# Optimization experiments

Hardware: AMD Instinct MI355X
Metric: run time of the kernel (lower is better)

## Reference

```python
import jax, jax.numpy as jnp
import numpy as np

K = 8            # tree arity
DEPTH = 7        # number of levels (0 = root)
N = (K**DEPTH - 1) // (K - 1)   # 299593 nodes, complete K-ary tree
D_EMB = 128
D_ENC = 128
D_DEC = 256


def _build_tree():
    idx = np.arange(N)
    offsets = (K**np.arange(DEPTH + 1) - 1) // (K - 1)  # level start offsets
    levels = np.searchsorted(offsets, idx, side='right') - 1
    parent = np.where(idx > 0, (idx - 1) // K, 0)       # heap layout
    return parent.astype(np.int64), levels.astype(np.int64)


def setup_inputs() -> dict:
    key = jax.random.key(0)
    ks = jax.random.split(key, 8)
    parent, levels = _build_tree()
    s = 0.05
    return {
        'x': jax.random.normal(ks[0], (N, D_EMB), jnp.float32),
        'parent': jnp.asarray(parent),
        'levels': jnp.asarray(levels),
        'num_levels': DEPTH,
        'W_iou': jax.random.normal(ks[1], (D_EMB, 3 * D_ENC), jnp.float32) * s,
        'b_iou': jnp.zeros((3 * D_ENC,), jnp.float32),
        'U_iou': jax.random.normal(ks[2], (D_ENC, 3 * D_ENC), jnp.float32) * s,
        'W_f': jax.random.normal(ks[3], (D_EMB, D_ENC), jnp.float32) * s,
        'b_f': jnp.zeros((D_ENC,), jnp.float32),
        'U_f': jax.random.normal(ks[4], (D_ENC, D_ENC), jnp.float32) * s,
        'W_out': jax.random.normal(ks[5], (D_ENC, D_DEC), jnp.float32) * s,
        'b_out': jnp.zeros((D_DEC,), jnp.float32),
        'ln_gamma': jnp.ones((D_DEC,), jnp.float32),
        'ln_beta': jnp.zeros((D_DEC,), jnp.float32),
    }


def _layer_norm(y, g, b, eps=1e-5):
    mu = jnp.mean(y, axis=-1, keepdims=True)
    var = jnp.var(y, axis=-1, keepdims=True)
    return (y - mu) * jax.lax.rsqrt(var + eps) * g + b


def reference(x, parent, levels, num_levels, W_iou, b_iou, U_iou, W_f, b_f, U_f, W_out, b_out, ln_gamma, ln_beta):
    n = x.shape[0]
    H = U_f.shape[0]
    # precomputed per-node input projections (dropout p=0 -> identity)
    x_iou = x @ W_iou + b_iou       # [N, 3H]
    x_f = x @ W_f + b_f             # [N, H]
    h = jnp.zeros((n, H), x.dtype)
    c = jnp.zeros((n, H), x.dtype)
    Uh_sum = jnp.zeros((n, 3 * H), x.dtype)
    fc_sum = jnp.zeros((n, H), x.dtype)
    # level-synchronous topological propagation: deepest level first
    for l in range(num_levels - 1, -1, -1):
        m = (levels == l)[:, None]
        # apply_node_func for nodes at level l
        iou = x_iou + Uh_sum
        i, o, u = jnp.split(iou, 3, axis=1)
        c_new = jax.nn.sigmoid(i) * jnp.tanh(u) + fc_sum
        h_new = jax.nn.sigmoid(o) * jnp.tanh(c_new)
        c = jnp.where(m, c_new, c)
        h = jnp.where(m, h_new, h)
        if l > 0:
            # message_func + reduce_func: gated child-state sums into parents
            mf = m.astype(x.dtype)
            f = jax.nn.sigmoid(x_f[parent] + h @ U_f)   # f uses dst x_f, src h
            Uh_sum = Uh_sum.at[parent].add((h @ U_iou) * mf)
            fc_sum = fc_sum.at[parent].add((c * f) * mf)
    return jnp.tanh(_layer_norm(h @ W_out + b_out, ln_gamma, ln_beta))
```

## Files before the change

kernel.cpp:

```cpp
#include <hip/hip_runtime.h>
#include <math.h>

#define DEV __device__ __forceinline__

#define NNODES 299593
#define NINTERNAL 37449

typedef __attribute__((ext_vector_type(8))) short short8;
typedef __attribute__((ext_vector_type(4))) float f32x4;

DEV float fsig(float x) { return 1.f / (1.f + __expf(-x)); }
DEV float ftanh(float x) { return 1.f - 2.f / (__expf(2.f * x) + 1.f); }

DEV unsigned short f2bf(float x) {
    unsigned int u = __float_as_uint(x);
    return (unsigned short)((u + 0x7fffu + ((u >> 16) & 1u)) >> 16);
}
DEV float bf2f(unsigned short h) { return __uint_as_float(((unsigned int)h) << 16); }

DEV f32x4 MF(short8 a, short8 b, f32x4 c) {
    return __builtin_amdgcn_mfma_f32_16x16x32_bf16(a, b, c, 0, 0, 0);
}

DEV short8 fragA(const short (*buf)[136], int r, int ks, int g) {
    return *reinterpret_cast<const short8*>(&buf[r][ks * 32 + g * 8]);
}

DEV void load8(float* v, const float* base, long row, int sc, int M) {
    if (row < M) {
        const float4* p4 = reinterpret_cast<const float4*>(base + row * 128 + sc);
        float4 a = p4[0], b = p4[1];
        v[0] = a.x; v[1] = a.y; v[2] = a.z; v[3] = a.w;
        v[4] = b.x; v[5] = b.y; v[6] = b.z; v[7] = b.w;
    } else {
#pragma unroll
        for (int e = 0; e < 8; ++e) v[e] = 0.f;
    }
}

DEV void stageHL(short (*H)[136], short (*L)[136], const float* v, int sr, int sc) {
    short8 vh, vl;
#pragma unroll
    for (int e = 0; e < 8; ++e) {
        unsigned short hb = f2bf(v[e]);
        vh[e] = (short)hb;
        vl[e] = (short)f2bf(v[e] - bf2f(hb));
    }
    *reinterpret_cast<short8*>(&H[sr][sc]) = vh;
    *reinterpret_cast<short8*>(&L[sr][sc]) = vl;
}

struct LvlP {
    const float* x;
    const float* hsum_in;
    const float* fc_in;
    const float* xf_par;
    unsigned short* h_out;
    float* hsum_out;
    float* fc_out;
    const float* Wiou;
    const float* biou;
    const float* Uiou;
    const float* Uf;
    long ntiles;
    int M;
};

template <bool UIOU, bool PAR>
__global__ __launch_bounds__(512) void lvl_kernel(LvlP p) {
    __shared__ __align__(16) short Ah[32][136];
    __shared__ __align__(16) short Al[32][136];
    __shared__ __align__(16) short Sh[UIOU ? 32 : 1][136];
    __shared__ __align__(16) short Sl[UIOU ? 32 : 1][136];
    __shared__ __align__(16) short Hs[32][136];

    const int tid = threadIdx.x;
    const int lane = tid & 63;
    const int w = tid >> 6;
    const int cl = lane & 15;
    const int g = lane >> 4;
    const int sr = tid >> 4;
    const int sc = (tid & 15) * 8;

    short8 Wh[4][3], Wl[4][3], Uh_[4][3], Ufh[4], Ufl[4];
    {
        const int colb = w * 16 + cl;
#pragma unroll
        for (int ks = 0; ks < 4; ++ks) {
#pragma unroll
            for (int f = 0; f < 3; ++f) {
#pragma unroll
                for (int e = 0; e < 8; ++e) {
                    float v = p.Wiou[(ks * 32 + g * 8 + e) * 384 + f * 128 + colb];
                    unsigned short hb = f2bf(v);
                    Wh[ks][f][e] = (short)hb;
                    Wl[ks][f][e] = (short)f2bf(v - bf2f(hb));
                }
                if constexpr (UIOU) {
#pragma unroll
                    for (int e = 0; e < 8; ++e)
                        Uh_[ks][f][e] = (short)f2bf(p.Uiou[(ks * 32 + g * 8 + e) * 384 + f * 128 + colb]);
                }
            }
            if constexpr (PAR) {
#pragma unroll
                for (int e = 0; e < 8; ++e) {
                    float v = p.Uf[(ks * 32 + g * 8 + e) * 128 + colb];
                    unsigned short hb = f2bf(v);
                    Ufh[ks][e] = (short)hb;
                    Ufl[ks][e] = (short)f2bf(v - bf2f(hb));
                }
            }
        }
    }

    long t = blockIdx.x;
    float va[8], sa[8];
    if (t < p.ntiles) {
        load8(va, p.x, t * 32 + sr, sc, p.M);
        if constexpr (UIOU) load8(sa, p.hsum_in, t * 32 + sr, sc, p.M);
    }

    for (; t < p.ntiles; t += gridDim.x) {
        const long row0 = t * 32;

        stageHL(Ah, Al, va, sr, sc);
        if constexpr (UIOU) stageHL(Sh, Sl, sa, sr, sc);
        __syncthreads();

        {
            long tn = t + gridDim.x;
            if (tn < p.ntiles) {
                load8(va, p.x, tn * 32 + sr, sc, p.M);
                if constexpr (UIOU) load8(sa, p.hsum_in, tn * 32 + sr, sc, p.M);
            }
        }

        f32x4 acc[2][3];
#pragma unroll
        for (int rf = 0; rf < 2; ++rf)
#pragma unroll
            for (int f = 0; f < 3; ++f) acc[rf][f] = (f32x4){0.f, 0.f, 0.f, 0.f};

#pragma unroll
        for (int ks = 0; ks < 4; ++ks)
#pragma unroll
            for (int rf = 0; rf < 2; ++rf) {
                short8 ah = fragA(Ah, rf * 16 + cl, ks, g);
                short8 al = fragA(Al, rf * 16 + cl, ks, g);
#pragma unroll
                for (int f = 0; f < 3; ++f) {
                    acc[rf][f] = MF(ah, Wh[ks][f], acc[rf][f]);
                    acc[rf][f] = MF(al, Wh[ks][f], acc[rf][f]);
                    acc[rf][f] = MF(ah, Wl[ks][f], acc[rf][f]);
                }
                if constexpr (UIOU) {
                    short8 sh = fragA(Sh, rf * 16 + cl, ks, g);
                    short8 sl = fragA(Sl, rf * 16 + cl, ks, g);
#pragma unroll
                    for (int f = 0; f < 3; ++f) {
                        acc[rf][f] = MF(sh, Uh_[ks][f], acc[rf][f]);
                        acc[rf][f] = MF(sl, Uh_[ks][f], acc[rf][f]);
                    }
                }
            }

        const int col = w * 16 + cl;
        float hreg[2][4], creg[2][4];
#pragma unroll
        for (int rf = 0; rf < 2; ++rf)
#pragma unroll
            for (int reg = 0; reg < 4; ++reg) {
                const long row = row0 + rf * 16 + g * 4 + reg;
                float hv = 0.f, cv = 0.f;
                if (row < p.M) {
                    float iv = acc[rf][0][reg] + p.biou[col];
                    float ov = acc[rf][1][reg] + p.biou[128 + col];
                    float uv = acc[rf][2][reg] + p.biou[256 + col];
                    float fcv = 0.f;
                    if constexpr (UIOU) fcv = p.fc_in[row * 128 + col];
                    cv = fsig(iv) * ftanh(uv) + fcv;
                    hv = bf2f(f2bf(fsig(ov) * ftanh(cv)));
                }
                hreg[rf][reg] = hv;
                creg[rf][reg] = cv;
                Hs[rf * 16 + g * 4 + reg][col] = (short)f2bf(hv);
            }
        __syncthreads();

        {
            const long row = row0 + sr;
            if (row < p.M)
                *reinterpret_cast<short8*>(p.h_out + row * 128 + sc) =
                    *reinterpret_cast<const short8*>(&Hs[sr][sc]);
        }

        if constexpr (PAR) {
            f32x4 acc2[2];
#pragma unroll
            for (int rf = 0; rf < 2; ++rf) acc2[rf] = (f32x4){0.f, 0.f, 0.f, 0.f};
#pragma unroll
            for (int ks = 0; ks < 4; ++ks)
#pragma unroll
                for (int rf = 0; rf < 2; ++rf) {
                    short8 hh = fragA(Hs, rf * 16 + cl, ks, g);
                    acc2[rf] = MF(hh, Ufh[ks], acc2[rf]);
                    acc2[rf] = MF(hh, Ufl[ks], acc2[rf]);
                }
#pragma unroll
            for (int rf = 0; rf < 2; ++rf) {
                float fcl = 0.f, hsl = 0.f;
#pragma unroll
                for (int reg = 0; reg < 4; ++reg) {
                    const long row = row0 + rf * 16 + g * 4 + reg;
                    if (row < p.M) {
                        float fpre = acc2[rf][reg] + p.xf_par[(row >> 3) * 128 + col];
                        fcl += fsig(fpre) * creg[rf][reg];
                    }
                    hsl += hreg[rf][reg];
                }
                fcl += __shfl_xor(fcl, 16);
                hsl += __shfl_xor(hsl, 16);
                const long grow = row0 + rf * 16 + (g >> 1) * 8;
                if (((g & 1) == 0) && grow < p.M) {
                    const long pr = grow >> 3;
                    p.fc_out[pr * 128 + col] = fcl;
                    p.hsum_out[pr * 128 + col] = hsl;
                }
            }
        }
    }
}

__global__ __launch_bounds__(512) void xf_kernel(const float* __restrict__ x,
                                                 const float* __restrict__ Wf,
                                                 const float* __restrict__ bf,
                                                 float* __restrict__ xf,
                                                 long ntiles, int M) {
    __shared__ __align__(16) short Ah[32][136];
    __shared__ __align__(16) short Al[32][136];
    const int tid = threadIdx.x;
    const int lane = tid & 63;
    const int w = tid >> 6;
    const int cl = lane & 15;
    const int g = lane >> 4;
    const int sr = tid >> 4;
    const int sc = (tid & 15) * 8;

    short8 Bh[4], Bl[4];
    {
        const int colb = w * 16 + cl;
#pragma unroll
        for (int ks = 0; ks < 4; ++ks)
#pragma unroll
            for (int e = 0; e < 8; ++e) {
                float v = Wf[(ks * 32 + g * 8 + e) * 128 + colb];
                unsigned short hb = f2bf(v);
                Bh[ks][e] = (short)hb;
                Bl[ks][e] = (short)f2bf(v - bf2f(hb));
            }
    }

    for (long t = blockIdx.x; t < ntiles; t += gridDim.x) {
        const long row0 = t * 32;
        float va[8];
        load8(va, x, row0 + sr, sc, M);
        stageHL(Ah, Al, va, sr, sc);
        __syncthreads();

        f32x4 acc[2];
#pragma unroll
        for (int rf = 0; rf < 2; ++rf) acc[rf] = (f32x4){0.f, 0.f, 0.f, 0.f};
#pragma unroll
        for (int ks = 0; ks < 4; ++ks)
#pragma unroll
            for (int rf = 0; rf < 2; ++rf) {
                short8 ah = fragA(Ah, rf * 16 + cl, ks, g);
                short8 al = fragA(Al, rf * 16 + cl, ks, g);
                acc[rf] = MF(ah, Bh[ks], acc[rf]);
                acc[rf] = MF(al, Bh[ks], acc[rf]);
                acc[rf] = MF(ah, Bl[ks], acc[rf]);
            }
        const int col = w * 16 + cl;
#pragma unroll
        for (int rf = 0; rf < 2; ++rf)
#pragma unroll
            for (int reg = 0; reg < 4; ++reg) {
                const long row = row0 + rf * 16 + g * 4 + reg;
                if (row < M) xf[row * 128 + col] = acc[rf][reg] + bf[col];
            }
        __syncthreads();
    }
}

struct LnP {
    const unsigned short* h;
    const float* Wout;
    const float* bout;
    const float* gam;
    const float* bet;
    float* out;
    long ntiles;
    int M;
};

__global__ __launch_bounds__(512) void ln_kernel(LnP p) {
    __shared__ __align__(16) short Hs[32][136];
    __shared__ float ob[32][257];
    __shared__ float2 red[8][2][4][4];

    const int tid = threadIdx.x;
    const int lane = tid & 63;
    const int w = tid >> 6;
    const int cl = lane & 15;
    const int g = lane >> 4;
    const int sr = tid >> 4;
    const int sc = (tid & 15) * 8;

    short8 Wh[4][2], Wl[4][2];
    {
#pragma unroll
        for (int ks = 0; ks < 4; ++ks)
#pragma unroll
            for (int f = 0; f < 2; ++f) {
                const int colb = f * 128 + w * 16 + cl;
#pragma unroll
                for (int e = 0; e < 8; ++e) {
                    float v = p.Wout[(ks * 32 + g * 8 + e) * 256 + colb];
                    unsigned short hb = f2bf(v);
                    Wh[ks][f][e] = (short)hb;
                    Wl[ks][f][e] = (short)f2bf(v - bf2f(hb));
                }
            }
    }

    long t = blockIdx.x;
    short8 hv = {0, 0, 0, 0, 0, 0, 0, 0};
    if (t < p.ntiles) {
        const long row = t * 32 + sr;
        if (row < p.M) hv = *reinterpret_cast<const short8*>(p.h + row * 128 + sc);
    }

    for (; t < p.ntiles; t += gridDim.x) {
        const long row0 = t * 32;
        *reinterpret_cast<short8*>(&Hs[sr][sc]) = hv;
        __syncthreads();

        {
            long tn = t + gridDim.x;
            if (tn < p.ntiles) {
                const long row = tn * 32 + sr;
                if (row < p.M) hv = *reinterpret_cast<const short8*>(p.h + row * 128 + sc);
                else           hv = (short8){0, 0, 0, 0, 0, 0, 0, 0};
            }
        }

        f32x4 acc[2][2];
#pragma unroll
        for (int rf = 0; rf < 2; ++rf)
#pragma unroll
            for (int f = 0; f < 2; ++f) acc[rf][f] = (f32x4){0.f, 0.f, 0.f, 0.f};
#pragma unroll
        for (int ks = 0; ks < 4; ++ks)
#pragma unroll
            for (int rf = 0; rf < 2; ++rf) {
                short8 hh = fragA(Hs, rf * 16 + cl, ks, g);
#pragma unroll
                for (int f = 0; f < 2; ++f) {
                    acc[rf][f] = MF(hh, Wh[ks][f], acc[rf][f]);
                    acc[rf][f] = MF(hh, Wl[ks][f], acc[rf][f]);
                }
            }

        float y[2][2][4];
#pragma unroll
        for (int rf = 0; rf < 2; ++rf)
#pragma unroll
            for (int f = 0; f < 2; ++f) {
                const int col = f * 128 + w * 16 + cl;
                const float bb = p.bout[col];
#pragma unroll
                for (int reg = 0; reg < 4; ++reg) y[rf][f][reg] = acc[rf][f][reg] + bb;
            }
#pragma unroll
        for (int rf = 0; rf < 2; ++rf) {
            float sp[4], qp[4];
#pragma unroll
            for (int reg = 0; reg < 4; ++reg) {
                float a = y[rf][0][reg], b = y[rf][1][reg];
                sp[reg] = a + b;
                qp[reg] = a * a + b * b;
            }
#pragma unroll
            for (int d = 1; d < 16; d <<= 1)
#pragma unroll
                for (int reg = 0; reg < 4; ++reg) {
                    sp[reg] += __shfl_xor(sp[reg], d);
                    qp[reg] += __shfl_xor(qp[reg], d);
                }
            if (cl == 0) {
#pragma unroll
                for (int reg = 0; reg < 4; ++reg)
                    red[w][rf][g][reg] = make_float2(sp[reg], qp[reg]);
            }
        }
        __syncthreads();

#pragma unroll
        for (int rf = 0; rf < 2; ++rf)
#pragma unroll
            for (int reg = 0; reg < 4; ++reg) {
                float s = 0.f, q = 0.f;
#pragma unroll
                for (int w2 = 0; w2 < 8; ++w2) {
                    float2 v = red[w2][rf][g][reg];
                    s += v.x;
                    q += v.y;
                }
                const float mu = s * (1.f / 256.f);
                const float var = q * (1.f / 256.f) - mu * mu;
                const float rstd = rsqrtf(var + 1e-5f);
                const int tr = rf * 16 + g * 4 + reg;
#pragma unroll
                for (int f = 0; f < 2; ++f) {
                    const int col = f * 128 + w * 16 + cl;
                    ob[tr][col] = ftanh((y[rf][f][reg] - mu) * rstd * p.gam[col] + p.bet[col]);
                }
            }
        __syncthreads();

        {
            const int r2 = tid >> 4;
            const int cc = tid & 15;
            const long row = row0 + r2;
            if (row < p.M) {
#pragma unroll
                for (int j = 0; j < 4; ++j) {
                    const int c0 = (j * 16 + cc) * 4;
                    float4 v;
                    v.x = ob[r2][c0];
                    v.y = ob[r2][c0 + 1];
                    v.z = ob[r2][c0 + 2];
                    v.w = ob[r2][c0 + 3];
                    *reinterpret_cast<float4*>(&p.out[row * 256 + c0]) = v;
                }
            }
        }
    }
}

extern "C" void kernel_launch(void* const* d_in, const int* in_sizes, int n_in,
                              void* d_out, int out_size, void* d_ws, size_t ws_size,
                              hipStream_t stream) {
    const float* x      = (const float*)d_in[0];
    const float* W_iou  = (const float*)d_in[4];
    const float* b_iou  = (const float*)d_in[5];
    const float* U_iou  = (const float*)d_in[6];
    const float* W_f    = (const float*)d_in[7];
    const float* b_f    = (const float*)d_in[8];
    const float* U_f    = (const float*)d_in[9];
    const float* W_out  = (const float*)d_in[10];
    const float* b_out  = (const float*)d_in[11];
    const float* ln_g   = (const float*)d_in[12];
    const float* ln_b   = (const float*)d_in[13];

    static const long OFF[8] = {0, 1, 9, 73, 585, 4681, 37449, 299593};

    char* ws = (char*)d_ws;
    unsigned short* h = (unsigned short*)ws;
    float* hsumA = (float*)(ws + 76695808L);
    float* hsumB = hsumA + 4194304L;
    float* fcA   = hsumB + 4194304L;
    float* fcB   = fcA + 4194304L;
    float* xf    = fcB + 4194304L;

    {
        long tiles = (NINTERNAL + 31) / 32;
        int grid = (int)(tiles < 512 ? tiles : 512);
        xf_kernel<<<grid, 512, 0, stream>>>(x, W_f, b_f, xf, tiles, NINTERNAL);
    }

    for (int l = 6; l >= 0; --l) {
        const long o = OFF[l];
        const int n = (int)(OFF[l + 1] - OFF[l]);
        const long tiles = (n + 31) / 32;
        const int grid = (int)(tiles < 512 ? tiles : 512);

        LvlP q = {};
        q.x = x + o * 128;
        q.h_out = h + o * 128;
        q.M = n;
        q.ntiles = tiles;
        q.Wiou = W_iou; q.biou = b_iou; q.Uiou = U_iou; q.Uf = U_f;
        if (l < 6) {
            q.hsum_in = (l & 1) ? hsumB : hsumA;
            q.fc_in   = (l & 1) ? fcB   : fcA;
        }
        if (l > 0) {
            q.hsum_out = ((l - 1) & 1) ? hsumB : hsumA;
            q.fc_out   = ((l - 1) & 1) ? fcB   : fcA;
            q.xf_par = xf + OFF[l - 1] * 128;
        }

        if (l == 6)      lvl_kernel<false, true ><<<grid, 512, 0, stream>>>(q);
        else if (l == 0) lvl_kernel<true,  false><<<grid, 512, 0, stream>>>(q);
        else             lvl_kernel<true,  true ><<<grid, 512, 0, stream>>>(q);
    }

    {
        LnP op = {};
        op.h = h; op.Wout = W_out; op.bout = b_out;
        op.gam = ln_g; op.bet = ln_b;
        op.out = (float*)d_out;
        op.ntiles = (NNODES + 31) / 32;
        op.M = NNODES;
        ln_kernel<<<512, 512, 0, stream>>>(op);
    }
}
```

Baseline: 1.074 ms.

## Pre-split weights once, drop low-weight MFMA terms, fuse top levels into one block

A new split_w kernel converts all weight matrices to bf16 fragments in an MFMA-friendly packed layout once, so the per-block fp32 weight loads and hi/lo splitting are gone. The third compensation MFMA (activation hi times weight lo) is removed in the W_iou, W_f and U_f products, trading a little accuracy for fewer matrix ops. The four smallest tree levels are fused into a single-block tail kernel that keeps the child sums in shared memory, replacing four tiny launches. Other changes: compile-time full-tile specialisation removes bounds checks, launch-bound occupancy hints are added, and fc/xf/bias loads are hoisted out of the inner loops.

New measurement: 881.5 us. -18.0%, faster.

```diff
diff --git a/kernel.cpp b/kernel.cpp
--- a/kernel.cpp
+++ b/kernel.cpp
@@ -1,4 +1,5 @@
 #include <hip/hip_runtime.h>
+#include <hip/hip_bf16.h>
 #include <math.h>
 
 #define DEV __device__ __forceinline__
@@ -12,11 +13,15 @@
 DEV float fsig(float x) { return 1.f / (1.f + __expf(-x)); }
 DEV float ftanh(float x) { return 1.f - 2.f / (__expf(2.f * x) + 1.f); }
 
-DEV unsigned short f2bf(float x) {
-    unsigned int u = __float_as_uint(x);
-    return (unsigned short)((u + 0x7fffu + ((u >> 16) & 1u)) >> 16);
-}
-DEV float bf2f(unsigned short h) { return __uint_as_float(((unsigned int)h) << 16); }
+DEV unsigned short f2bfu(float x) {
+    __hip_bfloat16 b = __float2bfloat16(x);
+    return *reinterpret_cast<unsigned short*>(&b);
+}
+DEV float bfuf(unsigned short u) {
+    __hip_bfloat16 b;
+    *reinterpret_cast<unsigned short*>(&b) = u;
+    return __bfloat162float(b);
+}
 
 DEV f32x4 MF(short8 a, short8 b, f32x4 c) {
     return __builtin_amdgcn_mfma_f32_16x16x32_bf16(a, b, c, 0, 0, 0);
@@ -26,8 +31,9 @@
     return *reinterpret_cast<const short8*>(&buf[r][ks * 32 + g * 8]);
 }
 
-DEV void load8(float* v, const float* base, long row, int sc, int M) {
-    if (row < M) {
+template <bool FULL>
+DEV void load8g(float* v, const float* base, long row, int sc, int M) {
+    if (FULL || row < M) {
         const float4* p4 = reinterpret_cast<const float4*>(base + row * 128 + sc);
         float4 a = p4[0], b = p4[1];
         v[0] = a.x; v[1] = a.y; v[2] = a.z; v[3] = a.w;
@@ -42,12 +48,35 @@
     short8 vh, vl;
 #pragma unroll
     for (int e = 0; e < 8; ++e) {
-        unsigned short hb = f2bf(v[e]);
+        unsigned short hb = f2bfu(v[e]);
         vh[e] = (short)hb;
-        vl[e] = (short)f2bf(v[e] - bf2f(hb));
+        vl[e] = (short)f2bfu(v[e] - bfuf(hb));
     }
     *reinterpret_cast<short8*>(&H[sr][sc]) = vh;
     *reinterpret_cast<short8*>(&L[sr][sc]) = vl;
+}
+
+struct SplitP {
+    const float *Wiou, *Uiou, *Uf, *Wout, *Wf;
+    unsigned short *WiH, *UiH, *UfH, *WoH, *WoL, *WfH;
+};
+__global__ __launch_bounds__(256) void split_w(SplitP s) {
+    int i = blockIdx.x * 256 + threadIdx.x;
+    const float* src;
+    unsigned short *oh, *ol = nullptr;
+    int W, base;
+    if (i < 49152)       { src = s.Wiou; W = 384; oh = s.WiH; ol = nullptr; base = 0; }
+    else if (i < 98304)  { src = s.Uiou; W = 384; oh = s.UiH; base = 49152; }
+    else if (i < 114688) { src = s.Uf;   W = 128; oh = s.UfH; base = 98304; }
+    else if (i < 147456) { src = s.Wout; W = 256; oh = s.WoH; ol = s.WoL; base = 114688; }
+    else                 { src = s.Wf;   W = 128; oh = s.WfH; base = 147456; }
+    int j = i - base;
+    int k = j / W, col = j - k * W;
+    float v = src[j];
+    unsigned short hb = f2bfu(v);
+    int po = ((k >> 5) * W + col) * 32 + (k & 31);
+    oh[po] = hb;
+    if (ol) ol[po] = f2bfu(v - bfuf(hb));
 }
 
 struct LvlP {
@@ -58,16 +87,16 @@
     unsigned short* h_out;
     float* hsum_out;
     float* fc_out;
-    const float* Wiou;
+    const unsigned short* WiH;
+    const unsigned short* UiH;
+    const unsigned short* UfH;
     const float* biou;
-    const float* Uiou;
-    const float* Uf;
     long ntiles;
     int M;
 };
 
-template <bool UIOU, bool PAR>
-__global__ __launch_bounds__(512) void lvl_kernel(LvlP p) {
+template <bool UIOU, bool PAR, bool FULL, int MINW>
+__global__ __launch_bounds__(512, MINW) void lvl_kernel(LvlP p) {
     __shared__ __align__(16) short Ah[32][136];
     __shared__ __align__(16) short Al[32][136];
     __shared__ __align__(16) short Sh[UIOU ? 32 : 1][136];
@@ -81,44 +110,25 @@
     const int g = lane >> 4;
     const int sr = tid >> 4;
     const int sc = (tid & 15) * 8;
-
-    short8 Wh[4][3], Wl[4][3], Uh_[4][3], Ufh[4], Ufl[4];
-    {
-        const int colb = w * 16 + cl;
-#pragma unroll
-        for (int ks = 0; ks < 4; ++ks) {
-#pragma unroll
-            for (int f = 0; f < 3; ++f) {
-#pragma unroll
-                for (int e = 0; e < 8; ++e) {
-                    float v = p.Wiou[(ks * 32 + g * 8 + e) * 384 + f * 128 + colb];
-                    unsigned short hb = f2bf(v);
-                    Wh[ks][f][e] = (short)hb;
-                    Wl[ks][f][e] = (short)f2bf(v - bf2f(hb));
-                }
-                if constexpr (UIOU) {
-#pragma unroll
-                    for (int e = 0; e < 8; ++e)
-                        Uh_[ks][f][e] = (short)f2bf(p.Uiou[(ks * 32 + g * 8 + e) * 384 + f * 128 + colb]);
-                }
-            }
-            if constexpr (PAR) {
-#pragma unroll
-                for (int e = 0; e < 8; ++e) {
-                    float v = p.Uf[(ks * 32 + g * 8 + e) * 128 + colb];
-                    unsigned short hb = f2bf(v);
-                    Ufh[ks][e] = (short)hb;
-                    Ufl[ks][e] = (short)f2bf(v - bf2f(hb));
-                }
-            }
-        }
-    }
+    const int col = w * 16 + cl;
+
+    short8 Wh[4][3];
+    short8 Uh[UIOU ? 4 : 1][UIOU ? 3 : 1];
+#pragma unroll
+    for (int ks = 0; ks < 4; ++ks)
+#pragma unroll
+        for (int f = 0; f < 3; ++f) {
+            Wh[ks][f] = *reinterpret_cast<const short8*>(&p.WiH[(ks * 384 + f * 128 + col) * 32 + g * 8]);
+            if constexpr (UIOU)
+                Uh[ks][f] = *reinterpret_cast<const short8*>(&p.UiH[(ks * 384 + f * 128 + col) * 32 + g * 8]);
+        }
+    const float bi = p.biou[col], bo = p.biou[128 + col], bu = p.biou[256 + col];
 
     long t = blockIdx.x;
     float va[8], sa[8];
     if (t < p.ntiles) {
-        load8(va, p.x, t * 32 + sr, sc, p.M);
-        if constexpr (UIOU) load8(sa, p.hsum_in, t * 32 + sr, sc, p.M);
+        load8g<FULL>(va, p.x, t * 32 + sr, sc, p.M);
+        if constexpr (UIOU) load8g<FULL>(sa, p.hsum_in, t * 32 + sr, sc, p.M);
     }
 
     for (; t < p.ntiles; t += gridDim.x) {
@@ -131,9 +141,19 @@
         {
             long tn = t + gridDim.x;
             if (tn < p.ntiles) {
-                load8(va, p.x, tn * 32 + sr, sc, p.M);
-                if constexpr (UIOU) load8(sa, p.hsum_in, tn * 32 + sr, sc, p.M);
-            }
+                load8g<FULL>(va, p.x, tn * 32 + sr, sc, p.M);
+                if constexpr (UIOU) load8g<FULL>(sa, p.hsum_in, tn * 32 + sr, sc, p.M);
+            }
+        }
+        float fcp[2][4];
+        if constexpr (UIOU) {
+#pragma unroll
+            for (int rf = 0; rf < 2; ++rf)
+#pragma unroll
+                for (int reg = 0; reg < 4; ++reg) {
+                    const long row = row0 + rf * 16 + g * 4 + reg;
+                    fcp[rf][reg] = (FULL || row < p.M) ? p.fc_in[row * 128 + col] : 0.f;
+                }
         }
 
         f32x4 acc[2][3];
@@ -152,20 +172,18 @@
                 for (int f = 0; f < 3; ++f) {
                     acc[rf][f] = MF(ah, Wh[ks][f], acc[rf][f]);
                     acc[rf][f] = MF(al, Wh[ks][f], acc[rf][f]);
-                    acc[rf][f] = MF(ah, Wl[ks][f], acc[rf][f]);
                 }
                 if constexpr (UIOU) {
                     short8 sh = fragA(Sh, rf * 16 + cl, ks, g);
                     short8 sl = fragA(Sl, rf * 16 + cl, ks, g);
 #pragma unroll
                     for (int f = 0; f < 3; ++f) {
-                        acc[rf][f] = MF(sh, Uh_[ks][f], acc[rf][f]);
-                        acc[rf][f] = MF(sl, Uh_[ks][f], acc[rf][f]);
+                        acc[rf][f] = MF(sh, Uh[ks][f], acc[rf][f]);
+                        acc[rf][f] = MF(sl, Uh[ks][f], acc[rf][f]);
                     }
                 }
             }
 
-        const int col = w * 16 + cl;
         float hreg[2][4], creg[2][4];
 #pragma unroll
         for (int rf = 0; rf < 2; ++rf)
@@ -173,56 +191,63 @@
             for (int reg = 0; reg < 4; ++reg) {
                 const long row = row0 + rf * 16 + g * 4 + reg;
                 float hv = 0.f, cv = 0.f;
-                if (row < p.M) {
-                    float iv = acc[rf][0][reg] + p.biou[col];
-                    float ov = acc[rf][1][reg] + p.biou[128 + col];
-                    float uv = acc[rf][2][reg] + p.biou[256 + col];
+                unsigned short hq = 0;
+                if (FULL || row < p.M) {
+                    float iv = acc[rf][0][reg] + bi;
+                    float ov = acc[rf][1][reg] + bo;
+                    float uv = acc[rf][2][reg] + bu;
                     float fcv = 0.f;
-                    if constexpr (UIOU) fcv = p.fc_in[row * 128 + col];
+                    if constexpr (UIOU) fcv = fcp[rf][reg];
                     cv = fsig(iv) * ftanh(uv) + fcv;
-                    hv = bf2f(f2bf(fsig(ov) * ftanh(cv)));
+                    hq = f2bfu(fsig(ov) * ftanh(cv));
+                    hv = bfuf(hq);
                 }
                 hreg[rf][reg] = hv;
                 creg[rf][reg] = cv;
-                Hs[rf * 16 + g * 4 + reg][col] = (short)f2bf(hv);
+                Hs[rf * 16 + g * 4 + reg][col] = (short)hq;
             }
         __syncthreads();
 
         {
-            const long row = row0 + sr;
-            if (row < p.M)
-                *reinterpret_cast<short8*>(p.h_out + row * 128 + sc) =
+            const long hrow = row0 + sr;
+            if (FULL || hrow < p.M)
+                *reinterpret_cast<short8*>(p.h_out + hrow * 128 + sc) =
                     *reinterpret_cast<const short8*>(&Hs[sr][sc]);
         }
 
         if constexpr (PAR) {
+            float xfp[2][4];
+#pragma unroll
+            for (int rf = 0; rf < 2; ++rf)
+#pragma unroll
+                for (int reg = 0; reg < 4; ++reg) {
+                    const long row = row0 + rf * 16 + g * 4 + reg;
+                    xfp[rf][reg] = (FULL || row < p.M) ? p.xf_par[(row >> 3) * 128 + col] : 0.f;
+                }
             f32x4 acc2[2];
 #pragma unroll
             for (int rf = 0; rf < 2; ++rf) acc2[rf] = (f32x4){0.f, 0.f, 0.f, 0.f};
 #pragma unroll
-            for (int ks = 0; ks < 4; ++ks)
-#pragma unroll
-                for (int rf = 0; rf < 2; ++rf) {
-                    short8 hh = fragA(Hs, rf * 16 + cl, ks, g);
-                    acc2[rf] = MF(hh, Ufh[ks], acc2[rf]);
-                    acc2[rf] = MF(hh, Ufl[ks], acc2[rf]);
-                }
+            for (int ks = 0; ks < 4; ++ks) {
+                short8 uf = *reinterpret_cast<const short8*>(&p.UfH[(ks * 128 + col) * 32 + g * 8]);
+#pragma unroll
+                for (int rf = 0; rf < 2; ++rf)
+                    acc2[rf] = MF(fragA(Hs, rf * 16 + cl, ks, g), uf, acc2[rf]);
+            }
 #pragma unroll
             for (int rf = 0; rf < 2; ++rf) {
                 float fcl = 0.f, hsl = 0.f;
 #pragma unroll
                 for (int reg = 0; reg < 4; ++reg) {
                     const long row = row0 + rf * 16 + g * 4 + reg;
-                    if (row < p.M) {
-                        float fpre = acc2[rf][reg] + p.xf_par[(row >> 3) * 128 + col];
-                        fcl += fsig(fpre) * creg[rf][reg];
-                    }
+                    if (FULL || row < p.M)
+                        fcl += fsig(acc2[rf][reg] + xfp[rf][reg]) * creg[rf][reg];
                     hsl += hreg[rf][reg];
                 }
                 fcl += __shfl_xor(fcl, 16);
                 hsl += __shfl_xor(hsl, 16);
                 const long grow = row0 + rf * 16 + (g >> 1) * 8;
-                if (((g & 1) == 0) && grow < p.M) {
+                if (((g & 1) == 0) && (FULL || grow < p.M)) {
                     const long pr = grow >> 3;
                     p.fc_out[pr * 128 + col] = fcl;
                     p.hsum_out[pr * 128 + col] = hsl;
@@ -232,11 +257,11 @@
     }
 }
 
-__global__ __launch_bounds__(512) void xf_kernel(const float* __restrict__ x,
-                                                 const float* __restrict__ Wf,
-                                                 const float* __restrict__ bf,
-                                                 float* __restrict__ xf,
-                                                 long ntiles, int M) {
+__global__ __launch_bounds__(512, 4) void xf_kernel(const float* __restrict__ x,
+                                                    const unsigned short* __restrict__ WfH,
+                                                    const float* __restrict__ bfv,
+                                                    float* __restrict__ xf,
+                                                    long ntiles, int M) {
     __shared__ __align__(16) short Ah[32][136];
     __shared__ __align__(16) short Al[32][136];
     const int tid = threadIdx.x;
@@ -246,28 +271,26 @@
     const int g = lane >> 4;
     const int sr = tid >> 4;
     const int sc = (tid & 15) * 8;
-
-    short8 Bh[4], Bl[4];
-    {
-        const int colb = w * 16 + cl;
-#pragma unroll
-        for (int ks = 0; ks < 4; ++ks)
-#pragma unroll
-            for (int e = 0; e < 8; ++e) {
-                float v = Wf[(ks * 32 + g * 8 + e) * 128 + colb];
-                unsigned short hb = f2bf(v);
-                Bh[ks][e] = (short)hb;
-                Bl[ks][e] = (short)f2bf(v - bf2f(hb));
-            }
-    }
-
-    for (long t = blockIdx.x; t < ntiles; t += gridDim.x) {
+    const int col = w * 16 + cl;
+
+    short8 Bh[4];
+#pragma unroll
+    for (int ks = 0; ks < 4; ++ks)
+        Bh[ks] = *reinterpret_cast<const short8*>(&WfH[(ks * 128 + col) * 32 + g * 8]);
+    const float bb = bfv[col];
+
+    long t = blockIdx.x;
+    float va[8];
+    if (t < ntiles) load8g<false>(va, x, t * 32 + sr, sc, M);
+
+    for (; t < ntiles; t += gridDim.x) {
         const long row0 = t * 32;
-        float va[8];
-        load8(va, x, row0 + sr, sc, M);
         stageHL(Ah, Al, va, sr, sc);
         __syncthreads();
-
+        {
+            long tn = t + gridDim.x;
+            if (tn < ntiles) load8g<false>(va, x, tn * 32 + sr, sc, M);
+        }
         f32x4 acc[2];
 #pragma unroll
         for (int rf = 0; rf < 2; ++rf) acc[rf] = (f32x4){0.f, 0.f, 0.f, 0.f};
@@ -279,23 +302,177 @@
                 short8 al = fragA(Al, rf * 16 + cl, ks, g);
                 acc[rf] = MF(ah, Bh[ks], acc[rf]);
                 acc[rf] = MF(al, Bh[ks], acc[rf]);
-                acc[rf] = MF(ah, Bl[ks], acc[rf]);
-            }
-        const int col = w * 16 + cl;
+            }
 #pragma unroll
         for (int rf = 0; rf < 2; ++rf)
 #pragma unroll
             for (int reg = 0; reg < 4; ++reg) {
                 const long row = row0 + rf * 16 + g * 4 + reg;
-                if (row < M) xf[row * 128 + col] = acc[rf][reg] + bf[col];
+                if (row < M) xf[row * 128 + col] = acc[rf][reg] + bb;
             }
         __syncthreads();
+    }
+}
+
+struct TailP {
+    const float* x;
+    const float* xf;
+    const float* hsum3;
+    const float* fc3;
+    unsigned short* h;
+    const unsigned short *WiH, *UiH, *UfH;
+    const float* biou;
+};
+
+__global__ __launch_bounds__(512, 1) void tail_kernel(TailP p) {
+    __shared__ __align__(16) short Ah[32][136];
+    __shared__ __align__(16) short Al[32][136];
+    __shared__ __align__(16) short Sh[32][136];
+    __shared__ __align__(16) short Sl[32][136];
+    __shared__ __align__(16) short Hs[32][136];
+    __shared__ float hsumL[64][128];
+    __shared__ float fcL[64][128];
+
+    const int tid = threadIdx.x;
+    const int lane = tid & 63;
+    const int w = tid >> 6;
+    const int cl = lane & 15;
+    const int g = lane >> 4;
+    const int sr = tid >> 4;
+    const int sc = (tid & 15) * 8;
+    const int col = w * 16 + cl;
+
+    short8 Wh[4][3], Uh[4][3], Uf[4];
+#pragma unroll
+    for (int ks = 0; ks < 4; ++ks) {
+#pragma unroll
+        for (int f = 0; f < 3; ++f) {
+            Wh[ks][f] = *reinterpret_cast<const short8*>(&p.WiH[(ks * 384 + f * 128 + col) * 32 + g * 8]);
+            Uh[ks][f] = *reinterpret_cast<const short8*>(&p.UiH[(ks * 384 + f * 128 + col) * 32 + g * 8]);
+        }
+        Uf[ks] = *reinterpret_cast<const short8*>(&p.UfH[(ks * 128 + col) * 32 + g * 8]);
+    }
+    const float bi = p.biou[col], bo = p.biou[128 + col], bu = p.biou[256 + col];
+
+    const int SZ[4] = {1, 8, 64, 512};
+    const long OFFS[4] = {0, 1, 9, 73};
+
+    for (int l = 3; l >= 0; --l) {
+        const int M = SZ[l];
+        const long o = OFFS[l];
+        const int tiles = (M + 31) / 32;
+        for (int t = 0; t < tiles; ++t) {
+            const long row0 = (long)t * 32;
+            float va[8];
+            load8g<false>(va, p.x + o * 128, row0 + sr, sc, M);
+            stageHL(Ah, Al, va, sr, sc);
+            float sa[8];
+            if (l == 3) {
+                load8g<false>(sa, p.hsum3, row0 + sr, sc, M);
+            } else {
+                const long r = row0 + sr;
+                if (r < M) {
+#pragma unroll
+                    for (int e = 0; e < 8; ++e) sa[e] = hsumL[r][sc + e];
+                } else {
+#pragma unroll
+                    for (int e = 0; e < 8; ++e) sa[e] = 0.f;
+                }
+            }
+            stageHL(Sh, Sl, sa, sr, sc);
+            __syncthreads();
+
+            f32x4 acc[2][3];
+#pragma unroll
+            for (int rf = 0; rf < 2; ++rf)
+#pragma unroll
+                for (int f = 0; f < 3; ++f) acc[rf][f] = (f32x4){0.f, 0.f, 0.f, 0.f};
+#pragma unroll
+            for (int ks = 0; ks < 4; ++ks)
+#pragma unroll
+                for (int rf = 0; rf < 2; ++rf) {
+                    short8 ah = fragA(Ah, rf * 16 + cl, ks, g);
+                    short8 al = fragA(Al, rf * 16 + cl, ks, g);
+                    short8 sh = fragA(Sh, rf * 16 + cl, ks, g);
+                    short8 sl = fragA(Sl, rf * 16 + cl, ks, g);
+#pragma unroll
+                    for (int f = 0; f < 3; ++f) {
+                        acc[rf][f] = MF(ah, Wh[ks][f], acc[rf][f]);
+                        acc[rf][f] = MF(al, Wh[ks][f], acc[rf][f]);
+                        acc[rf][f] = MF(sh, Uh[ks][f], acc[rf][f]);
+                        acc[rf][f] = MF(sl, Uh[ks][f], acc[rf][f]);
+                    }
+                }
+
+            float hreg[2][4], creg[2][4];
+#pragma unroll
+            for (int rf = 0; rf < 2; ++rf)
+#pragma unroll
+                for (int reg = 0; reg < 4; ++reg) {
+                    const long row = row0 + rf * 16 + g * 4 + reg;
+                    float hv = 0.f, cv = 0.f;
+                    unsigned short hq = 0;
+                    if (row < M) {
+                        float iv = acc[rf][0][reg] + bi;
+                        float ov = acc[rf][1][reg] + bo;
+                        float uv = acc[rf][2][reg] + bu;
+                        float fcv = (l == 3) ? p.fc3[row * 128 + col] : fcL[row][col];
+                        cv = fsig(iv) * ftanh(uv) + fcv;
+                        hq = f2bfu(fsig(ov) * ftanh(cv));
+                        hv = bfuf(hq);
+                    }
+                    hreg[rf][reg] = hv;
+                    creg[rf][reg] = cv;
+                    Hs[rf * 16 + g * 4 + reg][col] = (short)hq;
+                }
+            __syncthreads();
+
+            {
+                const long hrow = row0 + sr;
+                if (hrow < M)
+                    *reinterpret_cast<short8*>(p.h + (o + hrow) * 128 + sc) =
+                        *reinterpret_cast<const short8*>(&Hs[sr][sc]);
+            }
+
+            if (l > 0) {
+                const float* xfp_base = p.xf + OFFS[l - 1] * 128;
+                f32x4 acc2[2];
+#pragma unroll
+                for (int rf = 0; rf < 2; ++rf) acc2[rf] = (f32x4){0.f, 0.f, 0.f, 0.f};
+#pragma unroll
+                for (int ks = 0; ks < 4; ++ks)
+#pragma unroll
+                    for (int rf = 0; rf < 2; ++rf)
+                        acc2[rf] = MF(fragA(Hs, rf * 16 + cl, ks, g), Uf[ks], acc2[rf]);
+#pragma unroll
+                for (int rf = 0; rf < 2; ++rf) {
+                    float fcl = 0.f, hsl = 0.f;
+#pragma unroll
+                    for (int reg = 0; reg < 4; ++reg) {
+                        const long row = row0 + rf * 16 + g * 4 + reg;
+                        if (row < M)
+                            fcl += fsig(acc2[rf][reg] + xfp_base[(row >> 3) * 128 + col]) * creg[rf][reg];
+                        hsl += hreg[rf][reg];
+                    }
+                    fcl += __shfl_xor(fcl, 16);
+                    hsl += __shfl_xor(hsl, 16);
+                    const long grow = row0 + rf * 16 + (g >> 1) * 8;
+                    if (((g & 1) == 0) && grow < M) {
+                        const long pr = grow >> 3;
+                        fcL[pr][col] = fcl;
+                        hsumL[pr][col] = hsl;
+                    }
+                }
+            }
+            __syncthreads();
+        }
     }
 }
 
 struct LnP {
     const unsigned short* h;
-    const float* Wout;
+    const unsigned short* WoH;
+    const unsigned short* WoL;
     const float* bout;
     const float* gam;
     const float* bet;
@@ -304,7 +481,7 @@
     int M;
 };
 
-__global__ __launch_bounds__(512) void ln_kernel(LnP p) {
+__global__ __launch_bounds__(512, 4) void ln_kernel(LnP p) {
     __shared__ __align__(16) short Hs[32][136];
     __shared__ float ob[32][257];
     __shared__ float2 red[8][2][4][4];
@@ -316,23 +493,18 @@
     const int g = lane >> 4;
     const int sr = tid >> 4;
     const int sc = (tid & 15) * 8;
-
-    short8 Wh[4][2], Wl[4][2];
-    {
-#pragma unroll
-        for (int ks = 0; ks < 4; ++ks)
-#pragma unroll
-            for (int f = 0; f < 2; ++f) {
-                const int colb = f * 128 + w * 16 + cl;
-#pragma unroll
-                for (int e = 0; e < 8; ++e) {
-                    float v = p.Wout[(ks * 32 + g * 8 + e) * 256 + colb];
-                    unsigned short hb = f2bf(v);
-                    Wh[ks][f][e] = (short)hb;
-                    Wl[ks][f][e] = (short)f2bf(v - bf2f(hb));
-                }
-            }
-    }
+    const int col0 = w * 16 + cl;
+    const int col1 = 128 + col0;
+
+    short8 Wh[4][2];
+#pragma unroll
+    for (int ks = 0; ks < 4; ++ks)
+#pragma unroll
+        for (int f = 0; f < 2; ++f)
+            Wh[ks][f] = *reinterpret_cast<const short8*>(&p.WoH[(ks * 256 + f * 128 + col0) * 32 + g * 8]);
+    const float b0 = p.bout[col0], b1 = p.bout[col1];
+    const float g0 = p.gam[col0], g1 = p.gam[col1];
+    const float e0 = p.bet[col0], e1 = p.bet[col1];
 
     long t = blockIdx.x;
     short8 hv = {0, 0, 0, 0, 0, 0, 0, 0};
@@ -361,26 +533,26 @@
 #pragma unroll
             for (int f = 0; f < 2; ++f) acc[rf][f] = (f32x4){0.f, 0.f, 0.f, 0.f};
 #pragma unroll
-        for (int ks = 0; ks < 4; ++ks)
+        for (int ks = 0; ks < 4; ++ks) {
+            short8 wl0 = *reinterpret_cast<const short8*>(&p.WoL[(ks * 256 + col0) * 32 + g * 8]);
+            short8 wl1 = *reinterpret_cast<const short8*>(&p.WoL[(ks * 256 + col1) * 32 + g * 8]);
 #pragma unroll
             for (int rf = 0; rf < 2; ++rf) {
                 short8 hh = fragA(Hs, rf * 16 + cl, ks, g);
-#pragma unroll
-                for (int f = 0; f < 2; ++f) {
-                    acc[rf][f] = MF(hh, Wh[ks][f], acc[rf][f]);
-                    acc[rf][f] = MF(hh, Wl[ks][f], acc[rf][f]);
-                }
-            }
+                acc[rf][0] = MF(hh, Wh[ks][0], acc[rf][0]);
+                acc[rf][0] = MF(hh, wl0, acc[rf][0]);
+                acc[rf][1] = MF(hh, Wh[ks][1], acc[rf][1]);
+                acc[rf][1] = MF(hh, wl1, acc[rf][1]);
+            }
+        }
 
         float y[2][2][4];
 #pragma unroll
         for (int rf = 0; rf < 2; ++rf)
 #pragma unroll
-            for (int f = 0; f < 2; ++f) {
-                const int col = f * 128 + w * 16 + cl;
-                const float bb = p.bout[col];
-#pragma unroll
-                for (int reg = 0; reg < 4; ++reg) y[rf][f][reg] = acc[rf][f][reg] + bb;
+            for (int reg = 0; reg < 4; ++reg) {
+                y[rf][0][reg] = acc[rf][0][reg] + b0;
+                y[rf][1][reg] = acc[rf][1][reg] + b1;
             }
 #pragma unroll
         for (int rf = 0; rf < 2; ++rf) {
@@ -421,11 +593,8 @@
                 const float var = q * (1.f / 256.f) - mu * mu;
                 const float rstd = rsqrtf(var + 1e-5f);
                 const int tr = rf * 16 + g * 4 + reg;
-#pragma unroll
-                for (int f = 0; f < 2; ++f) {
-                    const int col = f * 128 + w * 16 + cl;
-                    ob[tr][col] = ftanh((y[rf][f][reg] - mu) * rstd * p.gam[col] + p.bet[col]);
-                }
+                ob[tr][col0] = ftanh((y[rf][0][reg] - mu) * rstd * g0 + e0);
+                ob[tr][col1] = ftanh((y[rf][1][reg] - mu) * rstd * g1 + e1);
             }
         __syncthreads();
 
@@ -469,48 +638,65 @@
     char* ws = (char*)d_ws;
     unsigned short* h = (unsigned short*)ws;
     float* hsumA = (float*)(ws + 76695808L);
-    float* hsumB = hsumA + 4194304L;
-    float* fcA   = hsumB + 4194304L;
-    float* fcB   = fcA + 4194304L;
-    float* xf    = fcB + 4194304L;
+    float* hsumB = (float*)(ws + 76695808L + 16777216L);
+    float* fcA   = (float*)(ws + 76695808L + 2 * 16777216L);
+    float* fcB   = (float*)(ws + 76695808L + 3 * 16777216L);
+    float* xf    = (float*)(ws + 76695808L + 4 * 16777216L);
+    unsigned short* wpk = (unsigned short*)(ws + 76695808L + 4 * 16777216L + 19173888L);
+    unsigned short* WiH = wpk;
+    unsigned short* UiH = WiH + 49152;
+    unsigned short* UfH = UiH + 49152;
+    unsigned short* WoH = UfH + 16384;
+    unsigned short* WoL = WoH + 32768;
+    unsigned short* WfH = WoL + 32768;
 
     {
-        long tiles = (NINTERNAL + 31) / 32;
-        int grid = (int)(tiles < 512 ? tiles : 512);
-        xf_kernel<<<grid, 512, 0, stream>>>(x, W_f, b_f, xf, tiles, NINTERNAL);
-    }
-
-    for (int l = 6; l >= 0; --l) {
-        const long o = OFF[l];
-        const int n = (int)(OFF[l + 1] - OFF[l]);
-        const long tiles = (n + 31) / 32;
-        const int grid = (int)(tiles < 512 ? tiles : 512);
-
+        SplitP sp = {W_iou, U_iou, U_f, W_out, W_f, WiH, UiH, UfH, WoH, WoL, WfH};
+        split_w<<<640, 256, 0, stream>>>(sp);
+    }
+
+    xf_kernel<<<512, 512, 0, stream>>>(x, WfH, b_f, xf, 1171, NINTERNAL);
+
+    {
         LvlP q = {};
-        q.x = x + o * 128;
-        q.h_out = h + o * 128;
-        q.M = n;
-        q.ntiles = tiles;
-        q.Wiou = W_iou; q.biou = b_iou; q.Uiou = U_iou; q.Uf = U_f;
-        if (l < 6) {
-            q.hsum_in = (l & 1) ? hsumB : hsumA;
-            q.fc_in   = (l & 1) ? fcB   : fcA;
-        }
-        if (l > 0) {
-            q.hsum_out = ((l - 1) & 1) ? hsumB : hsumA;
-            q.fc_out   = ((l - 1) & 1) ? fcB   : fcA;
-            q.xf_par = xf + OFF[l - 1] * 128;
-        }
-
-        if (l == 6)      lvl_kernel<false, true ><<<grid, 512, 0, stream>>>(q);
-        else if (l == 0) lvl_kernel<true,  false><<<grid, 512, 0, stream>>>(q);
-        else             lvl_kernel<true,  true ><<<grid, 512, 0, stream>>>(q);
-    }
-
+        q.x = x + OFF[6] * 128;
+        q.h_out = h + OFF[6] * 128;
+        q.hsum_out = hsumA; q.fc_out = fcA;
+        q.xf_par = xf + OFF[5] * 128;
+        q.WiH = WiH; q.UiH = UiH; q.UfH = UfH; q.biou = b_iou;
+        q.M = 262144; q.ntiles = 8192;
+        lvl_kernel<false, true, true, 4><<<512, 512, 0, stream>>>(q);
+    }
+    {
+        LvlP q = {};
+        q.x = x + OFF[5] * 128;
+        q.hsum_in = hsumA; q.fc_in = fcA;
+        q.h_out = h + OFF[5] * 128;
+        q.hsum_out = hsumB; q.fc_out = fcB;
+        q.xf_par = xf + OFF[4] * 128;
+        q.WiH = WiH; q.UiH = UiH; q.UfH = UfH; q.biou = b_iou;
+        q.M = 32768; q.ntiles = 1024;
+        lvl_kernel<true, true, true, 2><<<512, 512, 0, stream>>>(q);
+    }
+    {
+        LvlP q = {};
+        q.x = x + OFF[4] * 128;
+        q.hsum_in = hsumB; q.fc_in = fcB;
+        q.h_out = h + OFF[4] * 128;
+        q.hsum_out = hsumA; q.fc_out = fcA;
+        q.xf_par = xf + OFF[3] * 128;
+        q.WiH = WiH; q.UiH = UiH; q.UfH = UfH; q.biou = b_iou;
+        q.M = 4096; q.ntiles = 128;
+        lvl_kernel<true, true, true, 2><<<128, 512, 0, stream>>>(q);
+    }
+    {
+        TailP tp = {x, xf, hsumA, fcA, h, WiH, UiH, UfH, b_iou};
+        tail_kernel<<<1, 512, 0, stream>>>(tp);
+    }
     {
         LnP op = {};
-        op.h = h; op.Wout = W_out; op.bout = b_out;
-        op.gam = ln_g; op.bet = ln_b;
+        op.h = h; op.WoH = WoH; op.WoL = WoL;
+        op.bout = b_out; op.gam = ln_g; op.bet = ln_b;
         op.out = (float*)d_out;
         op.ntiles = (NNODES + 31) / 32;
         op.M = NNODES;
```
